# Performance work log

Hardware: AMD Instinct MI355X
Metric: run time of the kernel (lower is better)

## Reference

```python
import jax, jax.numpy as jnp
import numpy as np

B = 8          # graphs in batch
N = 10000      # nodes per graph
DEG = 16       # avg degree
F_IN = 128
H = 128
OUT = 64
RATIO = 0.5


def setup_inputs() -> dict:
    key = jax.random.key(0)
    ks = jax.random.split(key, 20)
    E = B * N * DEG
    x = jax.random.normal(ks[0], (B * N, F_IN), jnp.float32)
    gid = (jnp.arange(E, dtype=jnp.int32) // (N * DEG)) * N  # per-graph node offset
    src = jax.random.randint(ks[1], (E,), 0, N, jnp.int32) + gid
    dst = jax.random.randint(ks[2], (E,), 0, N, jnp.int32) + gid
    edge_index = jnp.stack([src, dst])

    def lin(k, fo, fi):
        return jax.random.normal(k, (fo, fi), jnp.float32) / np.sqrt(fi)

    return {
        "x": x,
        "edge_index": edge_index,
        "w1l_W": lin(ks[3], H, F_IN), "w1l_b": jnp.zeros((H,), jnp.float32),
        "w1r_W": lin(ks[4], H, F_IN),
        "pool1_w": jax.random.normal(ks[5], (H,), jnp.float32) / np.sqrt(H),
        "w2l_W": lin(ks[6], H, H), "w2l_b": jnp.zeros((H,), jnp.float32),
        "w2r_W": lin(ks[7], H, H),
        "pool2_w": jax.random.normal(ks[8], (H,), jnp.float32) / np.sqrt(H),
        "w3l_W": lin(ks[9], H, H), "w3l_b": jnp.zeros((H,), jnp.float32),
        "w3r_W": lin(ks[10], H, H),
        "pool3_w": jax.random.normal(ks[11], (H,), jnp.float32) / np.sqrt(H),
        "out_W": lin(ks[12], OUT, 2 * H), "out_b": jnp.zeros((OUT,), jnp.float32),
    }


def sage(x, src, dst, mask, Wl, bl, Wr, n_nodes):
    # PyG SAGEConv (mean aggr): lin_l(mean_{j->i} x_j) + lin_r(x_i); lin_l has bias.
    m = mask.astype(x.dtype)
    msg = x[src] * m[:, None]                                   # [E, F]
    agg = jax.ops.segment_sum(msg, dst, num_segments=n_nodes)   # [n, F]
    deg = jax.ops.segment_sum(m, dst, num_segments=n_nodes)     # [n]
    agg = agg / jnp.maximum(deg, 1.0)[:, None]                  # mean; empty -> 0
    return agg @ Wl.T + bl + x @ Wr.T


def topk_pool(x, src, dst, mask, w, n_per):
    # PyG TopKPooling: score = tanh(x.w / ||w||); keep top ceil(ratio*n) per graph;
    # x_out = x[perm] * score[perm]; edges filtered to surviving endpoints (masked here).
    k = int(np.ceil(RATIO * n_per))
    s = jnp.tanh((x @ w) / jnp.linalg.norm(w)).reshape(B, n_per)
    vals, idx = jax.lax.top_k(s, k)                             # [B, k]
    perm = (idx + (jnp.arange(B) * n_per)[:, None]).reshape(-1)  # global node ids
    x_new = x[perm] * vals.reshape(-1)[:, None]
    node_map = jnp.full((B * n_per,), -1, jnp.int32).at[perm].set(
        jnp.arange(B * k, dtype=jnp.int32))
    ns, nd = node_map[src], node_map[dst]
    valid = mask & (ns >= 0) & (nd >= 0)
    return x_new, jnp.where(valid, ns, 0), jnp.where(valid, nd, 0), valid, k


def summarize(x, k):
    xr = x.reshape(B, k, -1)
    return jnp.concatenate([xr.mean(axis=1), xr.max(axis=1)], axis=1)  # [B, 2H]


def reference(x, edge_index, w1l_W, w1l_b, w1r_W, pool1_w,
              w2l_W, w2l_b, w2r_W, pool2_w,
              w3l_W, w3l_b, w3r_W, pool3_w, out_W, out_b):
    src, dst = edge_index[0], edge_index[1]
    mask = jnp.ones(src.shape, bool)

    x = sage(x, src, dst, mask, w1l_W, w1l_b, w1r_W, B * N)
    x, src, dst, mask, k1 = topk_pool(x, src, dst, mask, pool1_w, N)
    s1 = summarize(x, k1)

    x = jax.nn.relu(sage(x, src, dst, mask, w2l_W, w2l_b, w2r_W, B * k1))
    x, src, dst, mask, k2 = topk_pool(x, src, dst, mask, pool2_w, k1)
    s2 = summarize(x, k2)

    x = sage(x, src, dst, mask, w3l_W, w3l_b, w3r_W, B * k2)
    x, src, dst, mask, k3 = topk_pool(x, src, dst, mask, pool3_w, k2)
    s3 = summarize(x, k3)

    summary = s1 + s2 + s3
    return summary @ out_W.T + out_b
```

## Files before the change

### kernel.cpp

```cpp
#include <hip/hip_runtime.h>
#include <hip/hip_bf16.h>
#include <math.h>

constexpr int B    = 8;
constexpr int NPG  = 10000;
constexpr int F    = 128;
constexpr int OUTD = 64;
constexpr int E    = B * NPG * 16;
constexpr int N0   = B * NPG;
constexpr int K1   = 5000, K2 = 2500, K3 = 1250;
constexpr int N1   = B * K1;
constexpr int N2   = B * K2;
constexpr int N3   = B * K3;
constexpr int PSPLIT = 256;
constexpr int ESH  = E / 8;
constexpr int KCH  = 32;
constexpr int CH   = ESH / KCH;

constexpr size_t OFF_IN   = 0;
constexpr size_t SZ_IN    = (size_t)N0 * 256 / 2;
constexpr size_t OFF_HB   = OFF_IN + SZ_IN;
constexpr size_t SZ_HB    = (size_t)N0 * F / 2;
constexpr size_t OFF_SC   = OFF_HB + SZ_HB;
constexpr size_t OFF_KEY  = OFF_SC + N0;
constexpr size_t OFF_MAP  = OFF_KEY + N0;
constexpr size_t OFF_MAP2 = OFF_MAP + N0;
constexpr size_t OFF_SEL1 = OFF_MAP2 + N1;
constexpr size_t OFF_SEL2 = OFF_SEL1 + N1;
constexpr size_t OFF_SEL3 = OFF_SEL2 + N2;
constexpr size_t OFF_SOC  = OFF_SEL3 + N3;
constexpr size_t OFF_VAL  = OFF_SOC + N2;
constexpr size_t OFF_CSR  = OFF_VAL + N1;
constexpr size_t OFF_HSUM = OFF_CSR + E;
constexpr size_t OFF_INCL = OFF_HSUM + N0;
constexpr size_t OFF_BSUM = OFF_INCL + N0;
constexpr size_t OFF_RS   = OFF_BSUM + 512;
constexpr size_t OFF_PART = OFF_RS + N0 + 64;
constexpr size_t OFF_SUM  = OFF_PART + (size_t)B * PSPLIT * 2 * F;
constexpr size_t OFF_WCAT = OFF_SUM + (size_t)B * 2 * F;
constexpr size_t OFF_MISC = OFF_WCAT + 3 * 128 * 256 / 2;

typedef __attribute__((ext_vector_type(8))) short short8;
typedef __attribute__((ext_vector_type(4))) float floatx4;

__device__ inline unsigned f2key(float f) {
    unsigned u = __float_as_uint(f);
    return (u & 0x80000000u) ? ~u : (u | 0x80000000u);
}
__device__ inline unsigned short f2b(float f) {
    unsigned u = __float_as_uint(f);
    return (unsigned short)((u + 0x7FFFu + ((u >> 16) & 1u)) >> 16);
}
__device__ inline float b2f(unsigned short u) {
    return __uint_as_float((unsigned)u << 16);
}
__device__ inline float blo(unsigned u) { return __uint_as_float(u << 16); }
__device__ inline float bhi(unsigned u) { return __uint_as_float(u & 0xFFFF0000u); }

__global__ void k_prep3(const float* __restrict__ Wl1, const float* __restrict__ Wr1,
                        const float* __restrict__ Wl2, const float* __restrict__ Wr2,
                        const float* __restrict__ Wl3, const float* __restrict__ Wr3,
                        const float* __restrict__ p1, const float* __restrict__ p2,
                        const float* __restrict__ p3,
                        unsigned short* __restrict__ wcat, float* __restrict__ normv) {
    int b = blockIdx.x;
    if (b == 96) {
        int t = threadIdx.x;
        int which = t >> 6, lane = t & 63;
        if (which < 3) {
            const float* pw = (which == 0) ? p1 : (which == 1) ? p2 : p3;
            float v = 0.0f;
            for (int j = lane; j < F; j += 64) { float a = pw[j]; v += a * a; }
            for (int o = 32; o > 0; o >>= 1) v += __shfl_down(v, o);
            if (lane == 0) normv[which] = sqrtf(v);
        }
        return;
    }
    int stage = b >> 5;
    const float* Wl = (stage == 0) ? Wl1 : (stage == 1) ? Wl2 : Wl3;
    const float* Wr = (stage == 0) ? Wr1 : (stage == 1) ? Wr2 : Wr3;
    unsigned short* W = wcat + (size_t)stage * 128 * 256;
    int idx = ((b & 31) * 256 + threadIdx.x) * 4;
    int o = idx >> 8, k = idx & 255;
    const float* p = (k < 128) ? (Wl + o * 128 + k) : (Wr + o * 128 + (k - 128));
    float4 v = *(const float4*)p;
    ushort4 u;
    u.x = f2b(v.x); u.y = f2b(v.y); u.z = f2b(v.z); u.w = f2b(v.w);
    *(ushort4*)(W + idx) = u;
}

__global__ void k_cvt(const float* __restrict__ x, unsigned short* __restrict__ IN, int n) {
    long t = blockIdx.x * (long)blockDim.x + threadIdx.x;
    int i = (int)(t >> 5), lane = (int)(t & 31);
    if (i >= n) return;
    float4 v = ((const float4*)(x + (size_t)i * F))[lane];
    ushort4 u;
    u.x = f2b(v.x); u.y = f2b(v.y); u.z = f2b(v.z); u.w = f2b(v.w);
    *(ushort4*)(IN + (size_t)i * 256 + 128 + lane * 4) = u;
}

__global__ __launch_bounds__(1024) void k_hist_p(const int* __restrict__ dst,
                                                 int* __restrict__ cnt) {
    __shared__ int h[NPG];
    int b = blockIdx.x, g = b & 7, k = b >> 3;
    for (int i = threadIdx.x; i < NPG; i += 1024) h[i] = 0;
    __syncthreads();
    int base = g * ESH + k * CH;
    for (int i = threadIdx.x; i < CH; i += 1024) {
        int d = __builtin_nontemporal_load(dst + base + i) - g * NPG;
        atomicAdd(&h[d], 1);
    }
    __syncthreads();
    int* o = cnt + (size_t)(g * KCH + k) * NPG;
    for (int i = threadIdx.x; i < NPG; i += 1024) o[i] = h[i];
}

__global__ __launch_bounds__(256) void k_scan1c(const int* __restrict__ cnt, int n,
                                                int* __restrict__ hsum,
                                                int* __restrict__ incl, int* __restrict__ bsum) {
    __shared__ int s[256];
    int i = blockIdx.x * 256 + threadIdx.x;
    int v = 0;
    if (i < n) {
        int g = i / NPG, l = i - g * NPG;
        const int* c = cnt + (size_t)g * KCH * NPG + l;
#pragma unroll
        for (int k = 0; k < KCH; k++) v += c[(size_t)k * NPG];
        hsum[i] = v;
    }
    s[threadIdx.x] = v;
    __syncthreads();
    for (int off = 1; off < 256; off <<= 1) {
        int t = s[threadIdx.x] + ((threadIdx.x >= off) ? s[threadIdx.x - off] : 0);
        __syncthreads();
        s[threadIdx.x] = t;
        __syncthreads();
    }
    if (i < n) incl[i] = s[threadIdx.x];
    if (threadIdx.x == 255) bsum[blockIdx.x] = s[255];
}

__global__ __launch_bounds__(512) void k_scan2(int* __restrict__ bsum, int nb) {
    __shared__ int s[512];
    int t = threadIdx.x;
    int v = (t < nb) ? bsum[t] : 0;
    s[t] = v;
    __syncthreads();
    for (int off = 1; off < 512; off <<= 1) {
        int u = s[t] + ((t >= off) ? s[t - off] : 0);
        __syncthreads();
        s[t] = u;
        __syncthreads();
    }
    if (t < nb) bsum[t] = s[t] - v;
}

__global__ void k_scan3c(const int* __restrict__ in, const int* __restrict__ incl,
                         const int* __restrict__ bsum, const int* __restrict__ cnt,
                         int* __restrict__ rowstart, int* __restrict__ cur0) {
    int i = blockIdx.x * 256 + threadIdx.x;
    if (i >= N0) return;
    int ex = incl[i] - in[i] + bsum[blockIdx.x];
    rowstart[i] = ex;
    if (i == N0 - 1) rowstart[N0] = ex + in[i];
    int g = i / NPG, l = i - g * NPG;
    const int* c = cnt + (size_t)g * KCH * NPG + l;
    int* u = cur0 + (size_t)g * KCH * NPG + l;
    int run = ex;
#pragma unroll
    for (int k = 0; k < KCH; k++) {
        u[(size_t)k * NPG] = run;
        run += c[(size_t)k * NPG];
    }
}

__global__ __launch_bounds__(1024) void k_csr_p(const int* __restrict__ src,
                                                const int* __restrict__ dst,
                                                const int* __restrict__ cur0,
                                                int* __restrict__ csr) {
    __shared__ int h[NPG];
    int b = blockIdx.x, g = b & 7, k = b >> 3;
    const int* u = cur0 + (size_t)(g * KCH + k) * NPG;
    for (int i = threadIdx.x; i < NPG; i += 1024) h[i] = u[i];
    __syncthreads();
    int base = g * ESH + k * CH;
    for (int i = threadIdx.x; i < CH; i += 1024) {
        int d = __builtin_nontemporal_load(dst + base + i) - g * NPG;
        int s = __builtin_nontemporal_load(src + base + i);
        int p = atomicAdd(&h[d], 1);
        csr[p] = s;
    }
}

__global__ void k_composechain(int* __restrict__ m1, const int* __restrict__ m2,
                               const int* __restrict__ s2, const int* __restrict__ s1,
                               int* __restrict__ soc, int n1, int n2) {
    int i = blockIdx.x * blockDim.x + threadIdx.x;
    if (i < n2) soc[i] = s1[s2[i]];
    if (i < n1) { int a = m1[i]; m1[i] = (a >= 0) ? m2[a] : -1; }
}

__global__ __launch_bounds__(256) void k_agg2b(unsigned short* __restrict__ IN,
                                               const int* __restrict__ rowstart,
                                               const int* __restrict__ csr, int npg) {
    int g = blockIdx.x & 7;
    int local = (blockIdx.x >> 3) * 16 + (threadIdx.x >> 4);
    int lane = threadIdx.x & 15;
    if (local >= npg) return;
    int i = g * npg + local;
    int b = rowstart[i], e = rowstart[i + 1];
    float a0 = 0, a1 = 0, a2 = 0, a3 = 0, a4 = 0, a5 = 0, a6 = 0, a7 = 0;
    int j = b;
    for (; j + 8 <= e; j += 8) {
        int sx[8];
#pragma unroll
        for (int t = 0; t < 8; t++) sx[t] = __builtin_nontemporal_load(csr + j + t);
        uint4 ux[8];
#pragma unroll
        for (int t = 0; t < 8; t++)
            ux[t] = *(const uint4*)(IN + (size_t)sx[t] * 256 + 128 + lane * 8);
#pragma unroll
        for (int t = 0; t < 8; t++) {
            a0 += blo(ux[t].x); a1 += bhi(ux[t].x);
            a2 += blo(ux[t].y); a3 += bhi(ux[t].y);
            a4 += blo(ux[t].z); a5 += bhi(ux[t].z);
            a6 += blo(ux[t].w); a7 += bhi(ux[t].w);
        }
    }
    for (; j < e; j++) {
        int s0 = __builtin_nontemporal_load(csr + j);
        uint4 u = *(const uint4*)(IN + (size_t)s0 * 256 + 128 + lane * 8);
        a0 += blo(u.x); a1 += bhi(u.x);
        a2 += blo(u.y); a3 += bhi(u.y);
        a4 += blo(u.z); a5 += bhi(u.z);
        a6 += blo(u.w); a7 += bhi(u.w);
    }
    float rd = 1.0f / fmaxf((float)(e - b), 1.0f);
    short8 o;
    o[0] = (short)f2b(a0 * rd); o[1] = (short)f2b(a1 * rd);
    o[2] = (short)f2b(a2 * rd); o[3] = (short)f2b(a3 * rd);
    o[4] = (short)f2b(a4 * rd); o[5] = (short)f2b(a5 * rd);
    o[6] = (short)f2b(a6 * rd); o[7] = (short)f2b(a7 * rd);
    *(short8*)(IN + (size_t)i * 256 + lane * 8) = o;
}

__global__ __launch_bounds__(256) void k_agg2m(unsigned short* __restrict__ IN,
                                               const int* __restrict__ rowstart,
                                               const int* __restrict__ csr,
                                               const int* __restrict__ map,
                                               const int* __restrict__ orig_of, int npg) {
    int g = blockIdx.x & 7;
    int local = (blockIdx.x >> 3) * 16 + (threadIdx.x >> 4);
    int lane = threadIdx.x & 15;
    if (local >= npg) return;
    int i = g * npg + local;
    int o = orig_of[i];
    int b = rowstart[o], e = rowstart[o + 1];
    float a0 = 0, a1 = 0, a2 = 0, a3 = 0, a4 = 0, a5 = 0, a6 = 0, a7 = 0;
    int d = 0;
    int j = b;
    for (; j + 4 <= e; j += 4) {
        int c0 = __builtin_nontemporal_load(csr + j);
        int c1 = __builtin_nontemporal_load(csr + j + 1);
        int c2 = __builtin_nontemporal_load(csr + j + 2);
        int c3 = __builtin_nontemporal_load(csr + j + 3);
        int m0 = map[c0], m1 = map[c1], m2 = map[c2], m3 = map[c3];
#pragma unroll
        for (int t = 0; t < 4; t++) {
            int s = (t == 0) ? m0 : (t == 1) ? m1 : (t == 2) ? m2 : m3;
            if (s >= 0) {
                uint4 u = *(const uint4*)(IN + (size_t)s * 256 + 128 + lane * 8);
                a0 += blo(u.x); a1 += bhi(u.x);
                a2 += blo(u.y); a3 += bhi(u.y);
                a4 += blo(u.z); a5 += bhi(u.z);
                a6 += blo(u.w); a7 += bhi(u.w);
                d++;
            }
        }
    }
    for (; j < e; j++) {
        int c0 = __builtin_nontemporal_load(csr + j);
        int s0 = map[c0];
        if (s0 >= 0) {
            uint4 u = *(const uint4*)(IN + (size_t)s0 * 256 + 128 + lane * 8);
            a0 += blo(u.x); a1 += bhi(u.x);
            a2 += blo(u.y); a3 += bhi(u.y);
            a4 += blo(u.z); a5 += bhi(u.z);
            a6 += blo(u.w); a7 += bhi(u.w);
            d++;
        }
    }
    float rd = 1.0f / fmaxf((float)d, 1.0f);
    short8 out;
    out[0] = (short)f2b(a0 * rd); out[1] = (short)f2b(a1 * rd);
    out[2] = (short)f2b(a2 * rd); out[3] = (short)f2b(a3 * rd);
    out[4] = (short)f2b(a4 * rd); out[5] = (short)f2b(a5 * rd);
    out[6] = (short)f2b(a6 * rd); out[7] = (short)f2b(a7 * rd);
    *(short8*)(IN + (size_t)i * 256 + lane * 8) = out;
}

__global__ __launch_bounds__(256) void k_sage_b(
    const unsigned short* __restrict__ IN, const unsigned short* __restrict__ Wcat,
    const float* __restrict__ bias, const float* __restrict__ poolw,
    const float* __restrict__ normv,
    unsigned short* __restrict__ hb, float* __restrict__ sc,
    unsigned* __restrict__ key, int npg, int relu) {
    __shared__ float lds[64][132];
    int tid = threadIdx.x;
    int wid = tid >> 6, lane = tid & 63;
    int q = lane >> 4, l15 = lane & 15;
    int g = blockIdx.x & 7, lb = blockIdx.x >> 3;
    int gbase = g * npg;
    int rowloc0 = lb * 128 + wid * 32;

    floatx4 acc0[8], acc1[8];
#pragma unroll
    for (int c = 0; c < 8; c++) {
        acc0[c] = (floatx4){0.f, 0.f, 0.f, 0.f};
        acc1[c] = (floatx4){0.f, 0.f, 0.f, 0.f};
    }

    const unsigned short* bbase = Wcat + (size_t)l15 * 256 + q * 8;
    int lr0 = min(rowloc0 + l15, npg - 1);
    int lr1 = min(rowloc0 + 16 + l15, npg - 1);
    const unsigned short* a0p = IN + (size_t)(gbase + lr0) * 256 + q * 8;
    const unsigned short* a1p = IN + (size_t)(gbase + lr1) * 256 + q * 8;
#pragma unroll
    for (int ks = 0; ks < 8; ks++) {
        short8 a0 = *(const short8*)(a0p + (ks << 5));
        short8 a1 = *(const short8*)(a1p + (ks << 5));
#pragma unroll
        for (int c = 0; c < 8; c++) {
            short8 b = *(const short8*)(bbase + (c << 12) + (ks << 5));
            acc0[c] = __builtin_amdgcn_mfma_f32_16x16x32_bf16(a0, b, acc0[c], 0, 0, 0);
            acc1[c] = __builtin_amdgcn_mfma_f32_16x16x32_bf16(a1, b, acc1[c], 0, 0, 0);
        }
    }

    float invn = 1.0f / (*normv);
#pragma unroll
    for (int t = 0; t < 2; t++) {
        float p0 = 0, p1 = 0, p2 = 0, p3 = 0;
#pragma unroll
        for (int c = 0; c < 8; c++) {
            int col = (c << 4) + l15;
            float bv = bias[col];
            float wv = poolw[col];
            floatx4 v = (t == 0) ? acc0[c] : acc1[c];
            v[0] += bv; v[1] += bv; v[2] += bv; v[3] += bv;
            if (relu) {
                v[0] = fmaxf(v[0], 0.f); v[1] = fmaxf(v[1], 0.f);
                v[2] = fmaxf(v[2], 0.f); v[3] = fmaxf(v[3], 0.f);
            }
            p0 += v[0] * wv; p1 += v[1] * wv; p2 += v[2] * wv; p3 += v[3] * wv;
            int lr = wid * 16 + q * 4;
            lds[lr + 0][col] = v[0];
            lds[lr + 1][col] = v[1];
            lds[lr + 2][col] = v[2];
            lds[lr + 3][col] = v[3];
        }
#pragma unroll
        for (int off = 1; off < 16; off <<= 1) {
            p0 += __shfl_xor(p0, off);
            p1 += __shfl_xor(p1, off);
            p2 += __shfl_xor(p2, off);
            p3 += __shfl_xor(p3, off);
        }
        if (l15 == 0) {
            float ps[4] = {p0, p1, p2, p3};
#pragma unroll
            for (int j = 0; j < 4; j++) {
                int lrow = rowloc0 + t * 16 + q * 4 + j;
                if (lrow < npg) {
                    float s = tanhf(ps[j] * invn);
                    sc[gbase + lrow] = s;
                    key[gbase + lrow] = f2key(s);
                }
            }
        }
        __syncthreads();
#pragma unroll
        for (int it = 0; it < 4; it++) {
            int task = it * 256 + tid;
            int r = task >> 4, grp = task & 15;
            int lrow = lb * 128 + (r >> 4) * 32 + t * 16 + (r & 15);
            if (lrow < npg) {
                float4 lo = *(const float4*)&lds[r][grp * 8];
                float4 hi = *(const float4*)&lds[r][grp * 8 + 4];
                short8 u;
                u[0] = (short)f2b(lo.x); u[1] = (short)f2b(lo.y);
                u[2] = (short)f2b(lo.z); u[3] = (short)f2b(lo.w);
                u[4] = (short)f2b(hi.x); u[5] = (short)f2b(hi.y);
                u[6] = (short)f2b(hi.z); u[7] = (short)f2b(hi.w);
                *(short8*)(hb + (size_t)(gbase + lrow) * 128 + grp * 8) = u;
            }
        }
        __syncthreads();
    }
}

__global__ __launch_bounds__(1024) void k_topk(
    const unsigned* __restrict__ keys, const float* __restrict__ sc,
    int n_per, int k,
    int* __restrict__ node_map, int* __restrict__ sel_old, float* __restrict__ vals) {
    int g = blockIdx.x, tid = threadIdx.x;
    int lane = tid & 63, wid = tid >> 6;
    const unsigned* kk = keys + (size_t)g * n_per;
    const float* ss = sc + (size_t)g * n_per;
    __shared__ int hist[256];
    __shared__ int suf[256];
    __shared__ unsigned sprefix;
    __shared__ int sr, sfound;
    __shared__ int we2[16], ws2[16];
    __shared__ int carry_pos, carry_eq;
    if (tid == 0) { sprefix = 0; sr = k; carry_pos = 0; carry_eq = 0; }
    __syncthreads();

    for (int b = 3; b >= 0; b--) {
        if (tid < 256) hist[tid] = 0;
        __syncthreads();
        unsigned pfx = sprefix;
        unsigned maskhi = (b == 3) ? 0u : (0xFFFFFFFFu << ((b + 1) * 8));
        for (int i = tid * 4; i < n_per; i += 4096) {
            uint4 kv4 = *(const uint4*)(kk + i);
#pragma unroll
            for (int j = 0; j < 4; j++) {
                unsigned kv = (j == 0) ? kv4.x : (j == 1) ? kv4.y : (j == 2) ? kv4.z : kv4.w;
                if ((kv & maskhi) == (pfx & maskhi))
                    atomicAdd(&hist[(kv >> (b * 8)) & 255], 1);
            }
        }
        __syncthreads();
        if (tid < 256) suf[tid] = hist[tid];
        __syncthreads();
        for (int off = 1; off < 256; off <<= 1) {
            int t = 0;
            if (tid < 256) t = suf[tid] + ((tid + off < 256) ? suf[tid + off] : 0);
            __syncthreads();
            if (tid < 256) suf[tid] = t;
            __syncthreads();
        }
        int r = sr;
        if (tid < 256) {
            int hi = (tid == 255) ? 0 : suf[tid + 1];
            if (hi < r && suf[tid] >= r) sfound = tid;
        }
        __syncthreads();
        if (tid == 0) {
            int v = sfound;
            int hi = (v == 255) ? 0 : suf[v + 1];
            sr = r - hi;
            sprefix = pfx | ((unsigned)v << (b * 8));
        }
        __syncthreads();
    }
    unsigned K = sprefix;
    int need = sr;
    __syncthreads();

    int nch = (n_per + 1023) >> 10;
    for (int ch = 0; ch < nch; ch++) {
        int i = (ch << 10) + tid;
        int valid = (i < n_per);
        unsigned kv = valid ? kk[i] : 0u;
        int is_gt = valid && (kv > K);
        int is_eq = valid && (kv == K);
        int e_incl = is_eq;
#pragma unroll
        for (int off = 1; off < 64; off <<= 1) {
            int t = __shfl_up(e_incl, off);
            e_incl += (lane >= off) ? t : 0;
        }
        if (lane == 63) we2[wid] = e_incl;
        __syncthreads();
        if (tid < 16) {
            int v = we2[tid];
#pragma unroll
            for (int off = 1; off < 16; off <<= 1) {
                int t = __shfl_up(v, off);
                v += ((int)tid >= off) ? t : 0;
            }
            we2[tid] = v;
        }
        __syncthreads();
        int eq_before = carry_eq + (e_incl - is_eq) + (wid ? we2[wid - 1] : 0);
        int sel = is_gt || (is_eq && eq_before < need);
        int s_incl = sel;
#pragma unroll
        for (int off = 1; off < 64; off <<= 1) {
            int t = __shfl_up(s_incl, off);
            s_incl += (lane >= off) ? t : 0;
        }
        if (lane == 63) ws2[wid] = s_incl;
        __syncthreads();
        if (tid < 16) {
            int v = ws2[tid];
#pragma unroll
            for (int off = 1; off < 16; off <<= 1) {
                int t = __shfl_up(v, off);
                v += ((int)tid >= off) ? t : 0;
            }
            ws2[tid] = v;
        }
        __syncthreads();
        int pos = carry_pos + (s_incl - sel) + (wid ? ws2[wid - 1] : 0);
        if (valid) {
            if (sel) {
                int ni = g * k + pos;
                node_map[(size_t)g * n_per + i] = ni;
                sel_old[ni] = g * n_per + i;
                vals[ni] = ss[i];
            } else {
                node_map[(size_t)g * n_per + i] = -1;
            }
        }
        __syncthreads();
        if (tid == 0) { carry_pos += ws2[15]; carry_eq += we2[15]; }
        __syncthreads();
    }
}

__global__ void k_gatherb(const unsigned short* __restrict__ hb,
                          const int* __restrict__ sel_old,
                          const float* __restrict__ vals,
                          unsigned short* __restrict__ INnext, int m) {
    long t = blockIdx.x * (long)blockDim.x + threadIdx.x;
    int i = (int)(t >> 5), lane = (int)(t & 31);
    if (i >= m) return;
    int oi = sel_old[i];
    float v = vals[i];
    ushort4 u = *(const ushort4*)(hb + (size_t)oi * 128 + lane * 4);
    ushort4 o;
    o.x = f2b(b2f(u.x) * v); o.y = f2b(b2f(u.y) * v);
    o.z = f2b(b2f(u.z) * v); o.w = f2b(b2f(u.w) * v);
    *(ushort4*)(INnext + (size_t)i * 256 + 128 + lane * 4) = o;
}

__global__ __launch_bounds__(64) void k_partial2(const unsigned short* __restrict__ IN,
                                                 int k, float* __restrict__ part) {
    int g = blockIdx.x >> 8, s = blockIdx.x & (PSPLIT - 1);
    int lane = threadIdx.x;
    int rows = (k + PSPLIT - 1) / PSPLIT;
    int r0 = s * rows, r1 = min(k, r0 + rows);
    float s0 = 0, s1 = 0, m0 = -INFINITY, m1 = -INFINITY;
    for (int r = r0; r < r1; r++) {
        ushort2 u = *(const ushort2*)(IN + (size_t)(g * k + r) * 256 + 128 + lane * 2);
        float v0 = b2f(u.x), v1 = b2f(u.y);
        s0 += v0; s1 += v1;
        m0 = fmaxf(m0, v0); m1 = fmaxf(m1, v1);
    }
    size_t base = ((size_t)(g * PSPLIT + s) * 2) * F;
    *(float2*)&part[base + lane * 2] = make_float2(s0, s1);
    *(float2*)&part[base + F + lane * 2] = make_float2(m0, m1);
}

__global__ __launch_bounds__(256) void k_sumreduce2(const float* __restrict__ part, int k,
                                                    float* __restrict__ summary, int accum) {
    int g = blockIdx.x;
    int half = threadIdx.x >> 7, f = threadIdx.x & 127;
    float sum = 0.0f, mx = -INFINITY;
    for (int s = 0; s < PSPLIT; s++) {
        float v = part[((size_t)(g * PSPLIT + s) * 2 + half) * F + f];
        sum += v;
        mx = fmaxf(mx, v);
    }
    float res = half ? mx : (sum / (float)k);
    int idx = g * 2 * F + half * F + f;
    if (accum) summary[idx] += res; else summary[idx] = res;
}

__global__ void k_out(const float* __restrict__ summary, const float* __restrict__ W,
                      const float* __restrict__ bias, float* __restrict__ out) {
    int g = blockIdx.x, j = threadIdx.x;
    float acc = bias[j];
    for (int t = 0; t < 2 * F; t++) acc += summary[g * 2 * F + t] * W[j * 2 * F + t];
    out[g * OUTD + j] = acc;
}

static inline int cdiv(long a, long b) { return (int)((a + b - 1) / b); }

extern "C" void kernel_launch(void* const* d_in, const int* in_sizes, int n_in,
                              void* d_out, int out_size, void* d_ws, size_t ws_size,
                              hipStream_t stream) {
    const float* x_in = (const float*)d_in[0];
    const int* ei     = (const int*)d_in[1];
    const float* w1lW = (const float*)d_in[2];
    const float* w1lb = (const float*)d_in[3];
    const float* w1rW = (const float*)d_in[4];
    const float* p1w  = (const float*)d_in[5];
    const float* w2lW = (const float*)d_in[6];
    const float* w2lb = (const float*)d_in[7];
    const float* w2rW = (const float*)d_in[8];
    const float* p2w  = (const float*)d_in[9];
    const float* w3lW = (const float*)d_in[10];
    const float* w3lb = (const float*)d_in[11];
    const float* w3rW = (const float*)d_in[12];
    const float* p3w  = (const float*)d_in[13];
    const float* outW = (const float*)d_in[14];
    const float* outb = (const float*)d_in[15];
    float* out = (float*)d_out;

    float* ws = (float*)d_ws;
    unsigned short* INb  = (unsigned short*)(ws + OFF_IN);
    unsigned short* hb   = (unsigned short*)(ws + OFF_HB);
    int* cnt     = (int*)(ws + OFF_HB);
    int* cur0    = cnt + (size_t)B * KCH * NPG;
    float* sc    = ws + OFF_SC;
    unsigned* key = (unsigned*)(ws + OFF_KEY);
    int* nmap1   = (int*)(ws + OFF_MAP);
    int* nmap2   = (int*)(ws + OFF_MAP2);
    int* selo1   = (int*)(ws + OFF_SEL1);
    int* selo2   = (int*)(ws + OFF_SEL2);
    int* selo3   = (int*)(ws + OFF_SEL3);
    int* soc     = (int*)(ws + OFF_SOC);
    float* vals  = ws + OFF_VAL;
    int* csr     = (int*)(ws + OFF_CSR);
    int* hsum    = (int*)(ws + OFF_HSUM);
    int* incl    = (int*)(ws + OFF_INCL);
    int* bsum    = (int*)(ws + OFF_BSUM);
    int* rs      = (int*)(ws + OFF_RS);
    float* part    = ws + OFF_PART;
    float* summary = ws + OFF_SUM;
    unsigned short* wcat = (unsigned short*)(ws + OFF_WCAT);
    int* misc_i  = (int*)(ws + OFF_MISC);
    float* normv = (float*)(misc_i + 20);

    const int* esrc = ei;
    const int* edst = ei + E;

    {
        int n = N0, nb = cdiv(n, 256);
        k_prep3<<<97, 256, 0, stream>>>(w1lW, w1rW, w2lW, w2rW, w3lW, w3rW,
                                        p1w, p2w, p3w, wcat, normv);
        k_cvt<<<cdiv((long)n * 32, 256), 256, 0, stream>>>(x_in, INb, n);
        k_hist_p<<<B * KCH, 1024, 0, stream>>>(edst, cnt);
        k_scan1c<<<nb, 256, 0, stream>>>(cnt, n, hsum, incl, bsum);
        k_scan2<<<1, 512, 0, stream>>>(bsum, nb);
        k_scan3c<<<nb, 256, 0, stream>>>(hsum, incl, bsum, cnt, rs, cur0);
        k_csr_p<<<B * KCH, 1024, 0, stream>>>(esrc, edst, cur0, csr);
        k_agg2b<<<8 * cdiv(NPG, 16), 256, 0, stream>>>(INb, rs, csr, NPG);
        k_sage_b<<<8 * cdiv(NPG, 128), 256, 0, stream>>>(INb, wcat, w1lb, p1w, normv,
                                                         hb, sc, key, NPG, 0);
        k_topk<<<B, 1024, 0, stream>>>(key, sc, NPG, K1, nmap1, selo1, vals);
        k_gatherb<<<cdiv((long)N1 * 32, 256), 256, 0, stream>>>(hb, selo1, vals, INb, N1);
        k_partial2<<<B * PSPLIT, 64, 0, stream>>>(INb, K1, part);
        k_sumreduce2<<<B, 256, 0, stream>>>(part, K1, summary, 0);
    }

    {
        k_agg2m<<<8 * cdiv(K1, 16), 256, 0, stream>>>(INb, rs, csr, nmap1, selo1, K1);
        k_sage_b<<<8 * cdiv(K1, 128), 256, 0, stream>>>(INb, wcat + 32768, w2lb, p2w, normv + 1,
                                                        hb, sc, key, K1, 1);
        k_topk<<<B, 1024, 0, stream>>>(key, sc, K1, K2, nmap2, selo2, vals);
        k_gatherb<<<cdiv((long)N2 * 32, 256), 256, 0, stream>>>(hb, selo2, vals, INb, N2);
        k_partial2<<<B * PSPLIT, 64, 0, stream>>>(INb, K2, part);
        k_sumreduce2<<<B, 256, 0, stream>>>(part, K2, summary, 1);
        k_composechain<<<cdiv(N0, 256), 256, 0, stream>>>(nmap1, nmap2, selo2, selo1, soc, N0, N2);
    }

    {
        k_agg2m<<<8 * cdiv(K2, 16), 256, 0, stream>>>(INb, rs, csr, nmap1, soc, K2);
        k_sage_b<<<8 * cdiv(K2, 128), 256, 0, stream>>>(INb, wcat + 65536, w3lb, p3w, normv + 2,
                                                        hb, sc, key, K2, 0);
        k_topk<<<B, 1024, 0, stream>>>(key, sc, K2, K3, nmap2, selo3, vals);
        k_gatherb<<<cdiv((long)N3 * 32, 256), 256, 0, stream>>>(hb, selo3, vals, INb, N3);
        k_partial2<<<B * PSPLIT, 64, 0, stream>>>(INb, K3, part);
        k_sumreduce2<<<B, 256, 0, stream>>>(part, K3, summary, 1);
    }

    k_out<<<B, OUTD, 0, stream>>>(summary, outW, outb, out);
}
```

Baseline: 364.7 us.

## Fuse neighbor mean-aggregation into SAGE GEMM via LDS tile and drop scan2

Merges the separate aggregation kernels into the SAGE matmul kernel. Each block gathers and averages neighbor features for its 128 rows into a swizzled LDS tile, which then feeds the MFMA loop directly. This avoids a global write and reread of the aggregated features and saves launches. The scan2 kernel is folded into scan3c by having each block reduce the preceding block sums. The gather kernel is widened to 16-byte loads. The cost is far fewer blocks doing the latency-bound gather, which may reduce memory-level parallelism.

Result: slower. 477.1 us (+30.8%).

```diff
diff --git a/kernel.cpp b/kernel.cpp
--- a/kernel.cpp
+++ b/kernel.cpp
@@ -140,27 +140,25 @@
     if (threadIdx.x == 255) bsum[blockIdx.x] = s[255];
 }
 
-__global__ __launch_bounds__(512) void k_scan2(int* __restrict__ bsum, int nb) {
-    __shared__ int s[512];
-    int t = threadIdx.x;
-    int v = (t < nb) ? bsum[t] : 0;
-    s[t] = v;
-    __syncthreads();
-    for (int off = 1; off < 512; off <<= 1) {
-        int u = s[t] + ((t >= off) ? s[t - off] : 0);
-        __syncthreads();
-        s[t] = u;
-        __syncthreads();
-    }
-    if (t < nb) bsum[t] = s[t] - v;
-}
-
-__global__ void k_scan3c(const int* __restrict__ in, const int* __restrict__ incl,
-                         const int* __restrict__ bsum, const int* __restrict__ cnt,
-                         int* __restrict__ rowstart, int* __restrict__ cur0) {
+__global__ __launch_bounds__(256) void k_scan3c(const int* __restrict__ in,
+                                                const int* __restrict__ incl,
+                                                const int* __restrict__ bsum,
+                                                const int* __restrict__ cnt,
+                                                int* __restrict__ rowstart,
+                                                int* __restrict__ cur0) {
+    __shared__ int red[256];
+    int acc = 0;
+    for (int t = threadIdx.x; t < blockIdx.x; t += 256) acc += bsum[t];
+    red[threadIdx.x] = acc;
+    __syncthreads();
+    for (int off = 128; off > 0; off >>= 1) {
+        if (threadIdx.x < off) red[threadIdx.x] += red[threadIdx.x + off];
+        __syncthreads();
+    }
+    int pref = red[0];
     int i = blockIdx.x * 256 + threadIdx.x;
     if (i >= N0) return;
-    int ex = incl[i] - in[i] + bsum[blockIdx.x];
+    int ex = incl[i] - in[i] + pref;
     rowstart[i] = ex;
     if (i == N0 - 1) rowstart[N0] = ex + in[i];
     int g = i / NPG, l = i - g * NPG;
@@ -200,117 +198,109 @@
     if (i < n1) { int a = m1[i]; m1[i] = (a >= 0) ? m2[a] : -1; }
 }
 
-__global__ __launch_bounds__(256) void k_agg2b(unsigned short* __restrict__ IN,
-                                               const int* __restrict__ rowstart,
-                                               const int* __restrict__ csr, int npg) {
-    int g = blockIdx.x & 7;
-    int local = (blockIdx.x >> 3) * 16 + (threadIdx.x >> 4);
-    int lane = threadIdx.x & 15;
-    if (local >= npg) return;
-    int i = g * npg + local;
-    int b = rowstart[i], e = rowstart[i + 1];
-    float a0 = 0, a1 = 0, a2 = 0, a3 = 0, a4 = 0, a5 = 0, a6 = 0, a7 = 0;
-    int j = b;
-    for (; j + 8 <= e; j += 8) {
-        int sx[8];
-#pragma unroll
-        for (int t = 0; t < 8; t++) sx[t] = __builtin_nontemporal_load(csr + j + t);
-        uint4 ux[8];
-#pragma unroll
-        for (int t = 0; t < 8; t++)
-            ux[t] = *(const uint4*)(IN + (size_t)sx[t] * 256 + 128 + lane * 8);
-#pragma unroll
-        for (int t = 0; t < 8; t++) {
-            a0 += blo(ux[t].x); a1 += bhi(ux[t].x);
-            a2 += blo(ux[t].y); a3 += bhi(ux[t].y);
-            a4 += blo(ux[t].z); a5 += bhi(ux[t].z);
-            a6 += blo(ux[t].w); a7 += bhi(ux[t].w);
-        }
-    }
-    for (; j < e; j++) {
-        int s0 = __builtin_nontemporal_load(csr + j);
-        uint4 u = *(const uint4*)(IN + (size_t)s0 * 256 + 128 + lane * 8);
-        a0 += blo(u.x); a1 += bhi(u.x);
-        a2 += blo(u.y); a3 += bhi(u.y);
-        a4 += blo(u.z); a5 += bhi(u.z);
-        a6 += blo(u.w); a7 += bhi(u.w);
-    }
-    float rd = 1.0f / fmaxf((float)(e - b), 1.0f);
-    short8 o;
-    o[0] = (short)f2b(a0 * rd); o[1] = (short)f2b(a1 * rd);
-    o[2] = (short)f2b(a2 * rd); o[3] = (short)f2b(a3 * rd);
-    o[4] = (short)f2b(a4 * rd); o[5] = (short)f2b(a5 * rd);
-    o[6] = (short)f2b(a6 * rd); o[7] = (short)f2b(a7 * rd);
-    *(short8*)(IN + (size_t)i * 256 + lane * 8) = o;
-}
-
-__global__ __launch_bounds__(256) void k_agg2m(unsigned short* __restrict__ IN,
-                                               const int* __restrict__ rowstart,
-                                               const int* __restrict__ csr,
-                                               const int* __restrict__ map,
-                                               const int* __restrict__ orig_of, int npg) {
-    int g = blockIdx.x & 7;
-    int local = (blockIdx.x >> 3) * 16 + (threadIdx.x >> 4);
-    int lane = threadIdx.x & 15;
-    if (local >= npg) return;
-    int i = g * npg + local;
-    int o = orig_of[i];
-    int b = rowstart[o], e = rowstart[o + 1];
-    float a0 = 0, a1 = 0, a2 = 0, a3 = 0, a4 = 0, a5 = 0, a6 = 0, a7 = 0;
-    int d = 0;
-    int j = b;
-    for (; j + 4 <= e; j += 4) {
-        int c0 = __builtin_nontemporal_load(csr + j);
-        int c1 = __builtin_nontemporal_load(csr + j + 1);
-        int c2 = __builtin_nontemporal_load(csr + j + 2);
-        int c3 = __builtin_nontemporal_load(csr + j + 3);
-        int m0 = map[c0], m1 = map[c1], m2 = map[c2], m3 = map[c3];
-#pragma unroll
-        for (int t = 0; t < 4; t++) {
-            int s = (t == 0) ? m0 : (t == 1) ? m1 : (t == 2) ? m2 : m3;
-            if (s >= 0) {
-                uint4 u = *(const uint4*)(IN + (size_t)s * 256 + 128 + lane * 8);
-                a0 += blo(u.x); a1 += bhi(u.x);
-                a2 += blo(u.y); a3 += bhi(u.y);
-                a4 += blo(u.z); a5 += bhi(u.z);
-                a6 += blo(u.w); a7 += bhi(u.w);
-                d++;
-            }
-        }
-    }
-    for (; j < e; j++) {
-        int c0 = __builtin_nontemporal_load(csr + j);
-        int s0 = map[c0];
-        if (s0 >= 0) {
-            uint4 u = *(const uint4*)(IN + (size_t)s0 * 256 + 128 + lane * 8);
-            a0 += blo(u.x); a1 += bhi(u.x);
-            a2 += blo(u.y); a3 += bhi(u.y);
-            a4 += blo(u.z); a5 += bhi(u.z);
-            a6 += blo(u.w); a7 += bhi(u.w);
-            d++;
-        }
-    }
-    float rd = 1.0f / fmaxf((float)d, 1.0f);
-    short8 out;
-    out[0] = (short)f2b(a0 * rd); out[1] = (short)f2b(a1 * rd);
-    out[2] = (short)f2b(a2 * rd); out[3] = (short)f2b(a3 * rd);
-    out[4] = (short)f2b(a4 * rd); out[5] = (short)f2b(a5 * rd);
-    out[6] = (short)f2b(a6 * rd); out[7] = (short)f2b(a7 * rd);
-    *(short8*)(IN + (size_t)i * 256 + lane * 8) = out;
-}
-
-__global__ __launch_bounds__(256) void k_sage_b(
-    const unsigned short* __restrict__ IN, const unsigned short* __restrict__ Wcat,
-    const float* __restrict__ bias, const float* __restrict__ poolw,
-    const float* __restrict__ normv,
+__global__ __launch_bounds__(256) void k_fuse(
+    const unsigned short* __restrict__ IN, const int* __restrict__ rowstart,
+    const int* __restrict__ csr, const int* __restrict__ map,
+    const int* __restrict__ orig_of,
+    const unsigned short* __restrict__ Wcat, const float* __restrict__ bias,
+    const float* __restrict__ poolw, const float* __restrict__ normv,
     unsigned short* __restrict__ hb, float* __restrict__ sc,
     unsigned* __restrict__ key, int npg, int relu) {
-    __shared__ float lds[64][132];
+    __shared__ unsigned char smem[64 * 132 * 4];
+    unsigned short* Am = (unsigned short*)smem;
+    float (*ep)[132] = (float(*)[132])smem;
     int tid = threadIdx.x;
+    int g = blockIdx.x & 7, lb = blockIdx.x >> 3;
+    int gbase = g * npg;
+
+    {
+        int sn = tid >> 4, lane = tid & 15;
+        for (int it = 0; it < 8; it++) {
+            int r = it * 16 + sn;
+            int lrow = lb * 128 + r;
+            float a0 = 0, a1 = 0, a2 = 0, a3 = 0, a4 = 0, a5 = 0, a6 = 0, a7 = 0;
+            float rd = 0.0f;
+            if (lrow < npg) {
+                int i = gbase + lrow;
+                int d = 0;
+                if (map) {
+                    int o = orig_of[i];
+                    int b = rowstart[o], e = rowstart[o + 1];
+                    int j = b;
+                    for (; j + 4 <= e; j += 4) {
+                        int c0 = __builtin_nontemporal_load(csr + j);
+                        int c1 = __builtin_nontemporal_load(csr + j + 1);
+                        int c2 = __builtin_nontemporal_load(csr + j + 2);
+                        int c3 = __builtin_nontemporal_load(csr + j + 3);
+                        int m0 = map[c0], m1 = map[c1], m2 = map[c2], m3 = map[c3];
+#pragma unroll
+                        for (int t = 0; t < 4; t++) {
+                            int s = (t == 0) ? m0 : (t == 1) ? m1 : (t == 2) ? m2 : m3;
+                            if (s >= 0) {
+                                uint4 u = *(const uint4*)(IN + (size_t)s * 256 + 128 + lane * 8);
+                                a0 += blo(u.x); a1 += bhi(u.x);
+                                a2 += blo(u.y); a3 += bhi(u.y);
+                                a4 += blo(u.z); a5 += bhi(u.z);
+                                a6 += blo(u.w); a7 += bhi(u.w);
+                                d++;
+                            }
+                        }
+                    }
+                    for (; j < e; j++) {
+                        int s = map[__builtin_nontemporal_load(csr + j)];
+                        if (s >= 0) {
+                            uint4 u = *(const uint4*)(IN + (size_t)s * 256 + 128 + lane * 8);
+                            a0 += blo(u.x); a1 += bhi(u.x);
+                            a2 += blo(u.y); a3 += bhi(u.y);
+                            a4 += blo(u.z); a5 += bhi(u.z);
+                            a6 += blo(u.w); a7 += bhi(u.w);
+                            d++;
+                        }
+                    }
+                } else {
+                    int b = rowstart[i], e = rowstart[i + 1];
+                    int j = b;
+                    for (; j + 8 <= e; j += 8) {
+                        int sx[8];
+#pragma unroll
+                        for (int t = 0; t < 8; t++) sx[t] = __builtin_nontemporal_load(csr + j + t);
+                        uint4 ux[8];
+#pragma unroll
+                        for (int t = 0; t < 8; t++)
+                            ux[t] = *(const uint4*)(IN + (size_t)sx[t] * 256 + 128 + lane * 8);
+#pragma unroll
+                        for (int t = 0; t < 8; t++) {
+                            a0 += blo(ux[t].x); a1 += bhi(ux[t].x);
+                            a2 += blo(ux[t].y); a3 += bhi(ux[t].y);
+                            a4 += blo(ux[t].z); a5 += bhi(ux[t].z);
+                            a6 += blo(ux[t].w); a7 += bhi(ux[t].w);
+                        }
+                    }
+                    for (; j < e; j++) {
+                        int s0 = __builtin_nontemporal_load(csr + j);
+                        uint4 u = *(const uint4*)(IN + (size_t)s0 * 256 + 128 + lane * 8);
+                        a0 += blo(u.x); a1 += bhi(u.x);
+                        a2 += blo(u.y); a3 += bhi(u.y);
+                        a4 += blo(u.z); a5 += bhi(u.z);
+                        a6 += blo(u.w); a7 += bhi(u.w);
+                    }
+                    d = e - b;
+                }
+                rd = 1.0f / fmaxf((float)d, 1.0f);
+            }
+            short8 o8;
+            o8[0] = (short)f2b(a0 * rd); o8[1] = (short)f2b(a1 * rd);
+            o8[2] = (short)f2b(a2 * rd); o8[3] = (short)f2b(a3 * rd);
+            o8[4] = (short)f2b(a4 * rd); o8[5] = (short)f2b(a5 * rd);
+            o8[6] = (short)f2b(a6 * rd); o8[7] = (short)f2b(a7 * rd);
+            int gr = lane ^ (r & 7);
+            *(short8*)(Am + (size_t)r * 128 + gr * 8) = o8;
+        }
+    }
+    __syncthreads();
+
     int wid = tid >> 6, lane = tid & 63;
     int q = lane >> 4, l15 = lane & 15;
-    int g = blockIdx.x & 7, lb = blockIdx.x >> 3;
-    int gbase = g * npg;
     int rowloc0 = lb * 128 + wid * 32;
 
     floatx4 acc0[8], acc1[8];
@@ -321,14 +311,24 @@
     }
 
     const unsigned short* bbase = Wcat + (size_t)l15 * 256 + q * 8;
+    int r0 = wid * 32 + l15;
+    int r1 = r0 + 16;
     int lr0 = min(rowloc0 + l15, npg - 1);
     int lr1 = min(rowloc0 + 16 + l15, npg - 1);
-    const unsigned short* a0p = IN + (size_t)(gbase + lr0) * 256 + q * 8;
-    const unsigned short* a1p = IN + (size_t)(gbase + lr1) * 256 + q * 8;
+    const unsigned short* x0p = IN + (size_t)(gbase + lr0) * 256 + 128 + q * 8;
+    const unsigned short* x1p = IN + (size_t)(gbase + lr1) * 256 + 128 + q * 8;
 #pragma unroll
     for (int ks = 0; ks < 8; ks++) {
-        short8 a0 = *(const short8*)(a0p + (ks << 5));
-        short8 a1 = *(const short8*)(a1p + (ks << 5));
+        short8 a0, a1;
+        if (ks < 4) {
+            int g0 = (ks * 4 + q) ^ (r0 & 7);
+            int g1 = (ks * 4 + q) ^ (r1 & 7);
+            a0 = *(const short8*)(Am + (size_t)r0 * 128 + g0 * 8);
+            a1 = *(const short8*)(Am + (size_t)r1 * 128 + g1 * 8);
+        } else {
+            a0 = *(const short8*)(x0p + ((ks - 4) << 5));
+            a1 = *(const short8*)(x1p + ((ks - 4) << 5));
+        }
 #pragma unroll
         for (int c = 0; c < 8; c++) {
             short8 b = *(const short8*)(bbase + (c << 12) + (ks << 5));
@@ -336,6 +336,7 @@
             acc1[c] = __builtin_amdgcn_mfma_f32_16x16x32_bf16(a1, b, acc1[c], 0, 0, 0);
         }
     }
+    __syncthreads();
 
     float invn = 1.0f / (*normv);
 #pragma unroll
@@ -354,10 +355,10 @@
             }
             p0 += v[0] * wv; p1 += v[1] * wv; p2 += v[2] * wv; p3 += v[3] * wv;
             int lr = wid * 16 + q * 4;
-            lds[lr + 0][col] = v[0];
-            lds[lr + 1][col] = v[1];
-            lds[lr + 2][col] = v[2];
-            lds[lr + 3][col] = v[3];
+            ep[lr + 0][col] = v[0];
+            ep[lr + 1][col] = v[1];
+            ep[lr + 2][col] = v[2];
+            ep[lr + 3][col] = v[3];
         }
 #pragma unroll
         for (int off = 1; off < 16; off <<= 1) {
@@ -385,8 +386,8 @@
             int r = task >> 4, grp = task & 15;
             int lrow = lb * 128 + (r >> 4) * 32 + t * 16 + (r & 15);
             if (lrow < npg) {
-                float4 lo = *(const float4*)&lds[r][grp * 8];
-                float4 hi = *(const float4*)&lds[r][grp * 8 + 4];
+                float4 lo = *(const float4*)&ep[r][grp * 8];
+                float4 hi = *(const float4*)&ep[r][grp * 8 + 4];
                 short8 u;
                 u[0] = (short)f2b(lo.x); u[1] = (short)f2b(lo.y);
                 u[2] = (short)f2b(lo.z); u[3] = (short)f2b(lo.w);
@@ -525,15 +526,17 @@
                           const float* __restrict__ vals,
                           unsigned short* __restrict__ INnext, int m) {
     long t = blockIdx.x * (long)blockDim.x + threadIdx.x;
-    int i = (int)(t >> 5), lane = (int)(t & 31);
+    int i = (int)(t >> 4), lane = (int)(t & 15);
     if (i >= m) return;
     int oi = sel_old[i];
     float v = vals[i];
-    ushort4 u = *(const ushort4*)(hb + (size_t)oi * 128 + lane * 4);
-    ushort4 o;
-    o.x = f2b(b2f(u.x) * v); o.y = f2b(b2f(u.y) * v);
-    o.z = f2b(b2f(u.z) * v); o.w = f2b(b2f(u.w) * v);
-    *(ushort4*)(INnext + (size_t)i * 256 + 128 + lane * 4) = o;
+    uint4 u = *(const uint4*)(hb + (size_t)oi * 128 + lane * 8);
+    short8 o;
+    o[0] = (short)f2b(blo(u.x) * v); o[1] = (short)f2b(bhi(u.x) * v);
+    o[2] = (short)f2b(blo(u.y) * v); o[3] = (short)f2b(bhi(u.y) * v);
+    o[4] = (short)f2b(blo(u.z) * v); o[5] = (short)f2b(bhi(u.z) * v);
+    o[6] = (short)f2b(blo(u.w) * v); o[7] = (short)f2b(bhi(u.w) * v);
+    *(short8*)(INnext + (size_t)i * 256 + 128 + lane * 8) = o;
 }
 
 __global__ __launch_bounds__(64) void k_partial2(const unsigned short* __restrict__ IN,
@@ -635,35 +638,34 @@
         k_cvt<<<cdiv((long)n * 32, 256), 256, 0, stream>>>(x_in, INb, n);
         k_hist_p<<<B * KCH, 1024, 0, stream>>>(edst, cnt);
         k_scan1c<<<nb, 256, 0, stream>>>(cnt, n, hsum, incl, bsum);
-        k_scan2<<<1, 512, 0, stream>>>(bsum, nb);
         k_scan3c<<<nb, 256, 0, stream>>>(hsum, incl, bsum, cnt, rs, cur0);
         k_csr_p<<<B * KCH, 1024, 0, stream>>>(esrc, edst, cur0, csr);
-        k_agg2b<<<8 * cdiv(NPG, 16), 256, 0, stream>>>(INb, rs, csr, NPG);
-        k_sage_b<<<8 * cdiv(NPG, 128), 256, 0, stream>>>(INb, wcat, w1lb, p1w, normv,
-                                                         hb, sc, key, NPG, 0);
+        k_fuse<<<8 * cdiv(NPG, 128), 256, 0, stream>>>(INb, rs, csr, nullptr, nullptr,
+                                                       wcat, w1lb, p1w, normv,
+                                                       hb, sc, key, NPG, 0);
         k_topk<<<B, 1024, 0, stream>>>(key, sc, NPG, K1, nmap1, selo1, vals);
-        k_gatherb<<<cdiv((long)N1 * 32, 256), 256, 0, stream>>>(hb, selo1, vals, INb, N1);
+        k_gatherb<<<cdiv((long)N1 * 16, 256), 256, 0, stream>>>(hb, selo1, vals, INb, N1);
         k_partial2<<<B * PSPLIT, 64, 0, stream>>>(INb, K1, part);
         k_sumreduce2<<<B, 256, 0, stream>>>(part, K1, summary, 0);
     }
 
     {
-        k_agg2m<<<8 * cdiv(K1, 16), 256, 0, stream>>>(INb, rs, csr, nmap1, selo1, K1);
-        k_sage_b<<<8 * cdiv(K1, 128), 256, 0, stream>>>(INb, wcat + 32768, w2lb, p2w, normv + 1,
-                                                        hb, sc, key, K1, 1);
+        k_fuse<<<8 * cdiv(K1, 128), 256, 0, stream>>>(INb, rs, csr, nmap1, selo1,
+                                                      wcat + 32768, w2lb, p2w, normv + 1,
+                                                      hb, sc, key, K1, 1);
         k_topk<<<B, 1024, 0, stream>>>(key, sc, K1, K2, nmap2, selo2, vals);
-        k_gatherb<<<cdiv((long)N2 * 32, 256), 256, 0, stream>>>(hb, selo2, vals, INb, N2);
+        k_gatherb<<<cdiv((long)N2 * 16, 256), 256, 0, stream>>>(hb, selo2, vals, INb, N2);
         k_partial2<<<B * PSPLIT, 64, 0, stream>>>(INb, K2, part);
         k_sumreduce2<<<B, 256, 0, stream>>>(part, K2, summary, 1);
         k_composechain<<<cdiv(N0, 256), 256, 0, stream>>>(nmap1, nmap2, selo2, selo1, soc, N0, N2);
     }
 
     {
-        k_agg2m<<<8 * cdiv(K2, 16), 256, 0, stream>>>(INb, rs, csr, nmap1, soc, K2);
-        k_sage_b<<<8 * cdiv(K2, 128), 256, 0, stream>>>(INb, wcat + 65536, w3lb, p3w, normv + 2,
-                                                        hb, sc, key, K2, 0);
+        k_fuse<<<8 * cdiv(K2, 128), 256, 0, stream>>>(INb, rs, csr, nmap1, soc,
+                                                      wcat + 65536, w3lb, p3w, normv + 2,
+                                                      hb, sc, key, K2, 0);
         k_topk<<<B, 1024, 0, stream>>>(key, sc, K2, K3, nmap2, selo3, vals);
-        k_gatherb<<<cdiv((long)N3 * 32, 256), 256, 0, stream>>>(hb, selo3, vals, INb, N3);
+        k_gatherb<<<cdiv((long)N3 * 16, 256), 256, 0, stream>>>(hb, selo3, vals, INb, N3);
         k_partial2<<<B * PSPLIT, 64, 0, stream>>>(INb, K3, part);
         k_sumreduce2<<<B, 256, 0, stream>>>(part, K3, summary, 1);
     }
```
